# Performance work log

Hardware: AMD Instinct MI355X
Metric: run time of the kernel (lower is better)

## Reference

```python
import jax, jax.numpy as jnp
import numpy as np

B = 16384
F = 1024
DELTA = 0.3
LAMB = 0.0005


def setup_inputs() -> dict:
    key = jax.random.key(0)
    k1, k2, k3, k4 = jax.random.split(key, 4)
    skt = jax.random.normal(k1, (B, F), dtype=jnp.float32)
    imgp = jax.random.normal(k2, (B, F), dtype=jnp.float32)
    imgn = jax.random.normal(k3, (B, F), dtype=jnp.float32)
    eye = jnp.eye(F, dtype=jnp.float32)
    w = eye + 0.05 * jax.random.normal(k4, (F, F), dtype=jnp.float32)
    return {"skt": skt, "imgp": imgp, "imgn": imgn, "w": w, "eye": eye}


def _distance(v1, v2, w, w_rowsum, w_colsum):
    # sum_{i,j} w[i,j] * (v1[:,i] - v2[:,j])**2
    #   = (v1**2) @ w.sum(1) - 2 * v1 @ w @ v2^T (diag) + (v2**2) @ w.sum(0)
    cross = ((v1 @ w) * v2).sum(axis=-1)  # [B]
    return (v1 * v1) @ w_rowsum - 2.0 * cross + (v2 * v2) @ w_colsum


def reference(skt, imgp, imgn, w, eye):
    w_rowsum = w.sum(axis=1)  # [F]
    w_colsum = w.sum(axis=0)  # [F]
    dp = _distance(skt, imgp, w, w_rowsum, w_colsum)  # [B]
    dn = _distance(skt, imgn, w, w_rowsum, w_colsum)  # [B]
    hinge = jnp.maximum(DELTA + dp - dn, 0.0).mean()
    dw = w - eye
    regu = jnp.abs(dw).sum() + jnp.sqrt((dw * dw).sum())
    return hinge + LAMB * regu
```

## Files before the change

kernel.cpp:

```cpp
#include <hip/hip_runtime.h>
#include <hip/hip_bf16.h>

#define FDIM 1024
#define BROWS 16384
#define DELTA_C 0.3f
#define LAMB_C 0.0005f

typedef __bf16 bf8v __attribute__((ext_vector_type(8)));
typedef float f4v __attribute__((ext_vector_type(4)));
typedef unsigned short u16;
typedef u16 u16x8 __attribute__((ext_vector_type(8)));

#define WS_PABS_OFF 4160
#define WS_PSQ_OFF 4672
#define WS_ROWACC_OFF 8192
#define WS_WB_OFF 131072
#define WS_SKTB_OFF (131072 + (1u << 21))
#define WS_NEED_FULL ((size_t)WS_SKTB_OFF + ((size_t)1 << 25))

__device__ __forceinline__ u16 f2bf(float f) {
  unsigned u = __builtin_bit_cast(unsigned, f);
  u += 0x7fffu + ((u >> 16) & 1u);
  return (u16)(u >> 16);
}

__device__ __forceinline__ void gload_lds16(const void* g, void* l) {
  __builtin_amdgcn_global_load_lds(
      (const __attribute__((address_space(1))) unsigned int*)g,
      (__attribute__((address_space(3))) unsigned int*)l, 16, 0, 0);
}

template <bool DO_A>
__global__ __launch_bounds__(256) void prep_all(const float* __restrict__ w,
                                                const float* __restrict__ skt,
                                                float* __restrict__ colsum,
                                                float* __restrict__ pabs,
                                                float* __restrict__ psq,
                                                u16* __restrict__ wb,
                                                u16* __restrict__ sktb) {
  __shared__ char smem_u[17440];
  const int t = threadIdx.x;
  const int bid = blockIdx.x;

  if (bid < 128) {
    u16(*tile)[1024] = (u16(*)[1024])smem_u;
    float* red = (float*)(smem_u + 16384);
    const int b = bid;
    const int k0 = b * 8;
    const int col = t * 4;

    float cs0 = 0.f, cs1 = 0.f, cs2 = 0.f, cs3 = 0.f;
    float aacc = 0.f, sacc = 0.f;
#pragma unroll
    for (int i = 0; i < 8; ++i) {
      const int gk = k0 + i;
      const float4 v = *(const float4*)(w + (size_t)gk * FDIM + col);
      ushort4 bb;
      bb.x = f2bf(v.x); bb.y = f2bf(v.y); bb.z = f2bf(v.z); bb.w = f2bf(v.w);
      *(ushort4*)(&tile[i][col]) = bb;
      cs0 += v.x; cs1 += v.y; cs2 += v.z; cs3 += v.w;
      const float d0 = v.x - (gk == col + 0 ? 1.f : 0.f);
      const float d1 = v.y - (gk == col + 1 ? 1.f : 0.f);
      const float d2 = v.z - (gk == col + 2 ? 1.f : 0.f);
      const float d3 = v.w - (gk == col + 3 ? 1.f : 0.f);
      aacc += fabsf(d0) + fabsf(d1) + fabsf(d2) + fabsf(d3);
      sacc += d0 * d0 + d1 * d1 + d2 * d2 + d3 * d3;
    }
    atomicAdd(&colsum[col + 0], cs0);
    atomicAdd(&colsum[col + 1], cs1);
    atomicAdd(&colsum[col + 2], cs2);
    atomicAdd(&colsum[col + 3], cs3);
#pragma unroll
    for (int off = 1; off < 64; off <<= 1) {
      aacc += __shfl_xor(aacc, off);
      sacc += __shfl_xor(sacc, off);
    }
    const int wid = t >> 6;
    if ((t & 63) == 0) { red[wid] = aacc; red[4 + wid] = sacc; }
    __syncthreads();
    if (t == 0) pabs[b] = red[0] + red[1] + red[2] + red[3];
    if (t == 1) psq[b] = red[4] + red[5] + red[6] + red[7];
#pragma unroll
    for (int j = 0; j < 4; ++j) {
      const int n = col + j;
      u16x8 pk;
#pragma unroll
      for (int e = 0; e < 8; ++e) pk[e] = tile[e][n];
      *(u16x8*)(wb + ((size_t)b * FDIM + n) * 8) = pk;
    }
  } else if constexpr (DO_A) {
    u16(*tile)[136] = (u16(*)[136])smem_u;
    const int ab = bid - 128;
    const int mb = ab >> 3;
    const int kb = ab & 7;
    const int m0 = mb * 64, k0 = kb * 128;
#pragma unroll
    for (int i = 0; i < 8; ++i) {
      const int fid = i * 256 + t;
      const int ml = fid >> 5;
      const int c4 = fid & 31;
      const float4 v = *(const float4*)(skt + (size_t)(m0 + ml) * FDIM + k0 + c4 * 4);
      ushort4 b;
      b.x = f2bf(v.x); b.y = f2bf(v.y); b.z = f2bf(v.z); b.w = f2bf(v.w);
      *(ushort4*)(&tile[ml][c4 * 4]) = b;
    }
    __syncthreads();
    const int ks0 = k0 >> 3;
#pragma unroll
    for (int i = 0; i < 4; ++i) {
      const int uid = i * 256 + t;
      const int si = uid >> 6;
      const int ml = uid & 63;
      const u16x8 pk = *(const u16x8*)(&tile[ml][si * 8]);
      *(u16x8*)(sktb + ((size_t)(ks0 + si) * BROWS + m0 + ml) * 8) = pk;
    }
  }
}

template <bool PRE>
__global__ __launch_bounds__(512, 4) void hofel_main(
    const float* __restrict__ skt, const float* __restrict__ imgp,
    const float* __restrict__ imgn, const u16* __restrict__ wb,
    const u16* __restrict__ sktb, const float* __restrict__ colsum,
    float* __restrict__ rowacc) {
  __shared__ u16 ldsT[2][12288];
  __shared__ float lds_cs[128];

  const int t = threadIdx.x;
  const int lane = t & 63;
  const int wid = t >> 6;
  const int l15 = lane & 15;
  const int l4 = lane >> 4;

  const int swz = (blockIdx.x & 7) * 64 + (blockIdx.x >> 3);
  const int mt = swz >> 3, nt = swz & 7;
  const int m0 = mt * 256, n0 = nt * 128;

  const int wr = wid >> 1, wc = wid & 1;
  const int wm = wr * 64, wn = wc * 64;

  f4v acc[4][4];
#pragma unroll
  for (int mi = 0; mi < 4; ++mi)
#pragma unroll
    for (int ni = 0; ni < 4; ++ni) {
      f4v z = {0.f, 0.f, 0.f, 0.f};
      acc[mi][ni] = z;
    }

  auto stage = [&](int buf, int kt) {
    if constexpr (PRE) {
#pragma unroll
      for (int r = 0; r < 3; ++r) {
        const int o = r * 8192 + wid * 1024;
        const int ol = o + lane * 16;
        const char* src;
        if (ol < 16384) {
          const int s = ol >> 12;
          const int m = (ol >> 4) & 255;
          src = (const char*)(sktb + ((size_t)(kt * 4 + s) * BROWS + m0 + m) * 8);
        } else {
          const int o2 = ol - 16384;
          const int s = o2 >> 11;
          const int n = (o2 >> 4) & 127;
          src = (const char*)(wb + ((size_t)(kt * 4 + s) * FDIM + n0 + n) * 8);
        }
        gload_lds16(src, (char*)ldsT[buf] + o);
      }
    } else {
      {
        const int o = wid * 1024;
        const int ol = o + lane * 16;
        const int s = ol >> 11;
        const int n = (ol >> 4) & 127;
        gload_lds16((const char*)(wb + ((size_t)(kt * 4 + s) * FDIM + n0 + n) * 8),
                    (char*)ldsT[buf] + 16384 + o);
      }
      const int m = t >> 1, h = t & 1;
      const float* ap = skt + (size_t)(m0 + m) * FDIM + kt * 32 + h * 16;
#pragma unroll
      for (int q = 0; q < 2; ++q) {
        const float4 v0 = *(const float4*)(ap + q * 8);
        const float4 v1 = *(const float4*)(ap + q * 8 + 4);
        u16x8 pk;
        pk[0] = f2bf(v0.x); pk[1] = f2bf(v0.y); pk[2] = f2bf(v0.z); pk[3] = f2bf(v0.w);
        pk[4] = f2bf(v1.x); pk[5] = f2bf(v1.y); pk[6] = f2bf(v1.z); pk[7] = f2bf(v1.w);
        *(u16x8*)((char*)ldsT[buf] + (h * 2 + q) * 4096 + m * 16) = pk;
      }
    }
  };

  stage(0, 0);
  if (t < 128) lds_cs[t] = colsum[n0 + t];
  __syncthreads();

  int cur = 0;
  for (int kt = 0; kt < 32; ++kt) {
    if (kt < 31) stage(cur ^ 1, kt + 1);

    const char* bufb = (const char*)ldsT[cur];
    bf8v aF[4], bF[4];
#pragma unroll
    for (int mi = 0; mi < 4; ++mi)
      aF[mi] = *(const bf8v*)(bufb + l4 * 4096 + (wm + mi * 16 + l15) * 16);
#pragma unroll
    for (int ni = 0; ni < 4; ++ni)
      bF[ni] = *(const bf8v*)(bufb + 16384 + l4 * 2048 + (wn + ni * 16 + l15) * 16);
#pragma unroll
    for (int mi = 0; mi < 4; ++mi)
#pragma unroll
      for (int ni = 0; ni < 4; ++ni)
        acc[mi][ni] = __builtin_amdgcn_mfma_f32_16x16x32_bf16(aF[mi], bF[ni], acc[mi][ni], 0, 0, 0);

    __syncthreads();
    cur ^= 1;
  }

#pragma unroll
  for (int mi = 0; mi < 4; ++mi) {
#pragma unroll
    for (int rr = 0; rr < 4; ++rr) {
      const int row = m0 + wm + mi * 16 + l4 * 4 + rr;
      const float* pr = imgp + (size_t)row * FDIM + n0;
      const float* nr = imgn + (size_t)row * FDIM + n0;
      float s = 0.f;
#pragma unroll
      for (int ni = 0; ni < 4; ++ni) {
        const int cl = wn + ni * 16 + l15;
        const float T = acc[mi][ni][rr];
        const float p = pr[cl];
        const float q = nr[cl];
        s += (p - q) * (-2.f * T + (p + q) * lds_cs[cl]);
      }
#pragma unroll
      for (int off = 1; off < 16; off <<= 1) s += __shfl_xor(s, off);
      if (l15 == 0) atomicAdd(rowacc + row, s);
    }
  }
}

__global__ __launch_bounds__(1024) void hinge_reduce(const float* __restrict__ rowacc,
                                                     float* __restrict__ wsf) {
  __shared__ float part[16];
  const int t = threadIdx.x;
  const int id = blockIdx.x * 1024 + t;
  float v = fmaxf(DELTA_C + rowacc[id], 0.f);
#pragma unroll
  for (int off = 1; off < 64; off <<= 1) v += __shfl_xor(v, off);
  if ((t & 63) == 0) part[t >> 6] = v;
  __syncthreads();
  if (t < 16) {
    float x = part[t];
#pragma unroll
    for (int off = 1; off < 16; off <<= 1) x += __shfl_xor(x, off);
    if (t == 0) atomicAdd(&wsf[0], x);
  }
}

__global__ __launch_bounds__(128) void finalize_k(const float* __restrict__ wsf,
                                                  const float* __restrict__ pabs,
                                                  const float* __restrict__ psq,
                                                  float* __restrict__ out) {
  __shared__ float ra[2], rs[2];
  const int t = threadIdx.x;
  float a = pabs[t], s = psq[t];
#pragma unroll
  for (int off = 1; off < 64; off <<= 1) {
    a += __shfl_xor(a, off);
    s += __shfl_xor(s, off);
  }
  if ((t & 63) == 0) { ra[t >> 6] = a; rs[t >> 6] = s; }
  __syncthreads();
  if (t == 0)
    out[0] = wsf[0] * (1.f / (float)BROWS) +
             LAMB_C * ((ra[0] + ra[1]) + sqrtf(rs[0] + rs[1]));
}

extern "C" void kernel_launch(void* const* d_in, const int* in_sizes, int n_in,
                              void* d_out, int out_size, void* d_ws, size_t ws_size,
                              hipStream_t stream) {
  const float* skt  = (const float*)d_in[0];
  const float* imgp = (const float*)d_in[1];
  const float* imgn = (const float*)d_in[2];
  const float* w    = (const float*)d_in[3];

  float* wsf = (float*)d_ws;
  float* colsum = wsf + 16;
  float* pabs = (float*)((char*)d_ws + WS_PABS_OFF);
  float* psq = (float*)((char*)d_ws + WS_PSQ_OFF);
  float* rowacc = (float*)((char*)d_ws + WS_ROWACC_OFF);
  u16* wb = (u16*)((char*)d_ws + WS_WB_OFF);
  u16* sktb = (u16*)((char*)d_ws + WS_SKTB_OFF);
  float* out = (float*)d_out;

  hipMemsetAsync(d_ws, 0, WS_ROWACC_OFF + BROWS * sizeof(float), stream);

  if (ws_size >= WS_NEED_FULL) {
    prep_all<true><<<128 + 2048, 256, 0, stream>>>(w, skt, colsum, pabs, psq, wb, sktb);
    hofel_main<true><<<512, 512, 0, stream>>>(skt, imgp, imgn, wb, sktb, colsum, rowacc);
  } else {
    prep_all<false><<<128, 256, 0, stream>>>(w, skt, colsum, pabs, psq, wb, sktb);
    hofel_main<false><<<512, 512, 0, stream>>>(skt, imgp, imgn, wb, sktb, colsum, rowacc);
  }

  hinge_reduce<<<16, 1024, 0, stream>>>(rowacc, wsf);
  finalize_k<<<1, 128, 0, stream>>>(wsf, pabs, psq, out);
}
```

Measured before the change: 87.64 us.

## Triple-buffer LDS with prefetch depth two and fine-grained vmcnt waits

Grows the shared-memory staging from two buffers to three and issues global-to-LDS loads two k-tiles ahead in the precomputed-bf16 path. A single raw s_barrier after a partial s_waitcnt vmcnt(3) replaces the full __syncthreads, so the next tile's loads stay in flight while the current tile runs on MFMA. The non-precomputed fallback becomes a simple single-buffer loop. LDS use goes from about 48KB to 72KB per block, which can cut resident blocks per CU.

```diff
diff --git a/kernel.cpp b/kernel.cpp
--- a/kernel.cpp
+++ b/kernel.cpp
@@ -123,7 +123,7 @@
     const float* __restrict__ imgn, const u16* __restrict__ wb,
     const u16* __restrict__ sktb, const float* __restrict__ colsum,
     float* __restrict__ rowacc) {
-  __shared__ u16 ldsT[2][12288];
+  __shared__ u16 ldsT[3][12288];
   __shared__ float lds_cs[128];
 
   const int t = threadIdx.x;
@@ -149,32 +149,80 @@
     }
 
   auto stage = [&](int buf, int kt) {
-    if constexpr (PRE) {
-#pragma unroll
-      for (int r = 0; r < 3; ++r) {
-        const int o = r * 8192 + wid * 1024;
-        const int ol = o + lane * 16;
-        const char* src;
-        if (ol < 16384) {
-          const int s = ol >> 12;
-          const int m = (ol >> 4) & 255;
-          src = (const char*)(sktb + ((size_t)(kt * 4 + s) * BROWS + m0 + m) * 8);
-        } else {
-          const int o2 = ol - 16384;
-          const int s = o2 >> 11;
-          const int n = (o2 >> 4) & 127;
-          src = (const char*)(wb + ((size_t)(kt * 4 + s) * FDIM + n0 + n) * 8);
-        }
-        gload_lds16(src, (char*)ldsT[buf] + o);
-      }
-    } else {
+#pragma unroll
+    for (int r = 0; r < 2; ++r) {
+      const int o = r * 8192 + wid * 1024;
+      const int ol = o + lane * 16;
+      const int s = ol >> 12;
+      const int m = (ol >> 4) & 255;
+      gload_lds16((const char*)(sktb + ((size_t)(kt * 4 + s) * BROWS + m0 + m) * 8),
+                  (char*)ldsT[buf] + o);
+    }
+    {
+      const int o2 = wid * 1024;
+      const int ol2 = o2 + lane * 16;
+      const int s = ol2 >> 11;
+      const int n = (ol2 >> 4) & 127;
+      gload_lds16((const char*)(wb + ((size_t)(kt * 4 + s) * FDIM + n0 + n) * 8),
+                  (char*)ldsT[buf] + 16384 + o2);
+    }
+  };
+
+  auto compute_tile = [&](int buf) {
+    const char* bufb = (const char*)ldsT[buf];
+    bf8v aF[4], bF[4];
+#pragma unroll
+    for (int mi = 0; mi < 4; ++mi)
+      aF[mi] = *(const bf8v*)(bufb + l4 * 4096 + (wm + mi * 16 + l15) * 16);
+#pragma unroll
+    for (int ni = 0; ni < 4; ++ni)
+      bF[ni] = *(const bf8v*)(bufb + 16384 + l4 * 2048 + (wn + ni * 16 + l15) * 16);
+#pragma unroll
+    for (int mi = 0; mi < 4; ++mi)
+#pragma unroll
+      for (int ni = 0; ni < 4; ++ni)
+        acc[mi][ni] = __builtin_amdgcn_mfma_f32_16x16x32_bf16(aF[mi], bF[ni], acc[mi][ni], 0, 0, 0);
+  };
+
+  if constexpr (PRE) {
+    if (t < 128) lds_cs[t] = colsum[n0 + t];
+    asm volatile("s_waitcnt vmcnt(0) lgkmcnt(0)" ::: "memory");
+    __builtin_amdgcn_sched_barrier(0);
+    stage(0, 0);
+    stage(1, 1);
+    asm volatile("s_waitcnt vmcnt(3)" ::: "memory");
+    __builtin_amdgcn_s_barrier();
+    __builtin_amdgcn_sched_barrier(0);
+
+    int cur = 0;
+    for (int kt = 0; kt < 32; ++kt) {
+      if (kt + 2 < 32) {
+        const int nb = (cur >= 1) ? cur - 1 : cur + 2;
+        stage(nb, kt + 2);
+      }
+      compute_tile(cur);
+      if (kt < 30) {
+        asm volatile("s_waitcnt vmcnt(3)" ::: "memory");
+        __builtin_amdgcn_s_barrier();
+        __builtin_amdgcn_sched_barrier(0);
+      } else if (kt == 30) {
+        asm volatile("s_waitcnt vmcnt(0)" ::: "memory");
+        __builtin_amdgcn_s_barrier();
+        __builtin_amdgcn_sched_barrier(0);
+      }
+      cur = (cur == 2) ? 0 : cur + 1;
+    }
+  } else {
+    if (t < 128) lds_cs[t] = colsum[n0 + t];
+    for (int kt = 0; kt < 32; ++kt) {
+      __syncthreads();
       {
-        const int o = wid * 1024;
-        const int ol = o + lane * 16;
-        const int s = ol >> 11;
-        const int n = (ol >> 4) & 127;
+        const int o2 = wid * 1024;
+        const int ol2 = o2 + lane * 16;
+        const int s = ol2 >> 11;
+        const int n = (ol2 >> 4) & 127;
         gload_lds16((const char*)(wb + ((size_t)(kt * 4 + s) * FDIM + n0 + n) * 8),
-                    (char*)ldsT[buf] + 16384 + o);
+                    (char*)ldsT[0] + 16384 + o2);
       }
       const int m = t >> 1, h = t & 1;
       const float* ap = skt + (size_t)(m0 + m) * FDIM + kt * 32 + h * 16;
@@ -185,35 +233,11 @@
         u16x8 pk;
         pk[0] = f2bf(v0.x); pk[1] = f2bf(v0.y); pk[2] = f2bf(v0.z); pk[3] = f2bf(v0.w);
         pk[4] = f2bf(v1.x); pk[5] = f2bf(v1.y); pk[6] = f2bf(v1.z); pk[7] = f2bf(v1.w);
-        *(u16x8*)((char*)ldsT[buf] + (h * 2 + q) * 4096 + m * 16) = pk;
-      }
-    }
-  };
-
-  stage(0, 0);
-  if (t < 128) lds_cs[t] = colsum[n0 + t];
-  __syncthreads();
-
-  int cur = 0;
-  for (int kt = 0; kt < 32; ++kt) {
-    if (kt < 31) stage(cur ^ 1, kt + 1);
-
-    const char* bufb = (const char*)ldsT[cur];
-    bf8v aF[4], bF[4];
-#pragma unroll
-    for (int mi = 0; mi < 4; ++mi)
-      aF[mi] = *(const bf8v*)(bufb + l4 * 4096 + (wm + mi * 16 + l15) * 16);
-#pragma unroll
-    for (int ni = 0; ni < 4; ++ni)
-      bF[ni] = *(const bf8v*)(bufb + 16384 + l4 * 2048 + (wn + ni * 16 + l15) * 16);
-#pragma unroll
-    for (int mi = 0; mi < 4; ++mi)
-#pragma unroll
-      for (int ni = 0; ni < 4; ++ni)
-        acc[mi][ni] = __builtin_amdgcn_mfma_f32_16x16x32_bf16(aF[mi], bF[ni], acc[mi][ni], 0, 0, 0);
-
-    __syncthreads();
-    cur ^= 1;
+        *(u16x8*)((char*)ldsT[0] + (h * 2 + q) * 4096 + m * 16) = pk;
+      }
+      __syncthreads();
+      compute_tile(0);
+    }
   }
 
 #pragma unroll
```

New measurement: 88.48 us. Within noise of the previous version (+1.0%).
